# Kernel optimization log

Measured on AMD Instinct MI355X. Metric: run time of the kernel, lower is better.

## Reference

```python
import jax, jax.numpy as jnp
import numpy as np

N = 100_000   # nodes
D = 128       # in_size == out_size
E = 800_000   # edges per etype
NE = 2        # number of edge types
H = 4         # num_heads
HD = D // H   # head size
EPS = 1e-5


def setup_inputs() -> dict:
    key = jax.random.key(0)
    ks = jax.random.split(key, 10)
    s = 0.05
    return {
        "feat": jax.random.normal(ks[0], (N, D), jnp.float32),
        "src": jax.random.randint(ks[1], (NE, E), 0, N, dtype=jnp.int32),
        "dst": jax.random.randint(ks[2], (NE, E), 0, N, dtype=jnp.int32),
        # per-etype Linear weights stored [in, out] so y = x @ W + b (torch stores transposed)
        "Wt": jax.random.normal(ks[3], (NE, D, D), jnp.float32) * s,
        "bt": jnp.zeros((NE, D), jnp.float32),
        "Kw": jax.random.normal(ks[4], (NE, D, D), jnp.float32) * s,
        "Kb": jnp.zeros((NE, D), jnp.float32),
        "Qw": jax.random.normal(ks[5], (NE, D, D), jnp.float32) * s,
        "Qb": jnp.zeros((NE, D), jnp.float32),
        "Vw": jax.random.normal(ks[6], (NE, D, D), jnp.float32) * s,
        "Vb": jnp.zeros((NE, D), jnp.float32),
        "ln_g": jnp.ones((D,), jnp.float32),
        "ln_b": jnp.zeros((D,), jnp.float32),
    }


def _attn(Wh, kw, kb, qw, qb, vw, vb):
    # per-node multi-head attention ACROSS HEADS: attn is [N, H, H] (faithful to bmm in torch code)
    k = (Wh @ kw + kb).reshape(-1, H, HD)
    q = (Wh @ qw + qb).reshape(-1, H, HD)
    v = (Wh @ vw + vb).reshape(-1, H, HD)
    scores = jnp.einsum('nhd,ngd->nhg', q, k) / np.float32(np.sqrt(HD))
    a = jax.nn.softmax(scores, axis=2)  # dropout is identity in eval
    return jnp.einsum('nhg,ngd->nhd', a, v).reshape(-1, D)


def reference(feat, src, dst, Wt, bt, Kw, Kb, Qw, Qb, Vw, Vb, ln_g, ln_b):
    h = jnp.zeros_like(feat)
    ones_e = jnp.ones((E,), feat.dtype)
    for e in range(NE):  # small fixed loop over edge types
        Wh = _attn(feat @ Wt[e] + bt[e], Kw[e], Kb[e], Qw[e], Qb[e], Vw[e], Vb[e])
        msg = Wh[src[e]]                                      # copy_u: [E, D]
        tot = jax.ops.segment_sum(msg, dst[e], num_segments=N)
        deg = jax.ops.segment_sum(ones_e, dst[e], num_segments=N)
        h = h + tot / jnp.maximum(deg, 1.0)[:, None]          # mean (0 for isolated), cross-etype 'sum'
    h = h + feat  # identity residual (in_size == out_size)
    mu = jnp.mean(h, axis=-1, keepdims=True)
    var = jnp.mean((h - mu) ** 2, axis=-1, keepdims=True)
    return (h - mu) / jnp.sqrt(var + EPS) * ln_g + ln_b  # LayerNorm; dropout identity in eval
```

## Files before the change

### kernel.cpp

```cpp
#include <hip/hip_runtime.h>
#include <hip/hip_bf16.h>
#include <stdint.h>

#define D 128
#define NET 2
#define CAP 32

typedef __bf16 bf16x8 __attribute__((ext_vector_type(8)));
typedef float f32x4 __attribute__((ext_vector_type(4)));
typedef short s16x8 __attribute__((ext_vector_type(8)));
typedef unsigned short us16x8 __attribute__((ext_vector_type(8)));

__device__ __forceinline__ float b2f(unsigned short u) {
  return __builtin_bit_cast(float, ((uint32_t)u) << 16);
}
__device__ __forceinline__ unsigned short f2b(float f) {
  __hip_bfloat16 h = __float2bfloat16(f);
  return __builtin_bit_cast(unsigned short, h);
}

__global__ void k_combine(const float* __restrict__ Wt, const float* __restrict__ bt,
                          const float* __restrict__ Kw, const float* __restrict__ Kb,
                          const float* __restrict__ Qw, const float* __restrict__ Qb,
                          const float* __restrict__ Vw, const float* __restrict__ Vb,
                          unsigned short* __restrict__ WTc, float* __restrict__ bc) {
  int combo = blockIdx.y;
  int et = combo / 3, which = combo % 3;
  const float* W0 = Wt + (size_t)et * D * D;
  const float* W1 = ((which == 0) ? Kw : (which == 1) ? Qw : Vw) + (size_t)et * D * D;
  const float* b1 = ((which == 0) ? Kb : (which == 1) ? Qb : Vb) + (size_t)et * D;
  const float* b0 = bt + (size_t)et * D;

  int t = threadIdx.x;
  int i = blockIdx.x * 16 + (t >> 4);
  int jb = (t & 15) * 8;
  float acc[8];
#pragma unroll
  for (int j = 0; j < 8; j++) acc[j] = 0.f;
  for (int k = 0; k < D; k++) {
    float a0 = W0[(size_t)i * D + k];
    const float* w1p = W1 + (size_t)k * D + jb;
#pragma unroll
    for (int j = 0; j < 8; j++) acc[j] += a0 * w1p[j];
  }
  unsigned short* wout = WTc + (size_t)combo * D * D;
#pragma unroll
  for (int j = 0; j < 8; j++) wout[(size_t)(jb + j) * D + i] = f2b(acc[j]);

  if (blockIdx.x == 0 && t < D) {
    float s = b1[t];
    for (int k = 0; k < D; k++) s += b0[k] * W1[(size_t)k * D + t];
    bc[(size_t)combo * D + t] = s;
  }
}

__device__ __forceinline__ void stage_w(const unsigned short* __restrict__ W,
                                        unsigned short (*Ws)[136], int tid) {
  int r = tid >> 1, hh = tid & 1;
  const us16x8* gp = (const us16x8*)(W + (size_t)r * D + hh * 64);
  us16x8* lp = (us16x8*)&Ws[r][hh * 64];
#pragma unroll
  for (int i = 0; i < 8; i++) lp[i] = gp[i];
}

__device__ __forceinline__ void load_pf(const unsigned short* __restrict__ W,
                                        us16x8* pf, int sr, int sh) {
  const us16x8* gp = (const us16x8*)(W + (size_t)sr * D + sh * 64);
#pragma unroll
  for (int i = 0; i < 8; i++) pf[i] = gp[i];
}

__device__ __forceinline__ void write_pf(const us16x8* pf, unsigned short (*Ws)[136],
                                         int sr, int sh) {
  us16x8* lp = (us16x8*)&Ws[sr][sh * 64];
#pragma unroll
  for (int i = 0; i < 8; i++) lp[i] = pf[i];
}

__device__ __forceinline__ void gemm_frag(const bf16x8* af, unsigned short (*Ws)[136],
                                          int m, int q, f32x4* acc) {
#pragma unroll
  for (int nt = 0; nt < 8; nt++) {
    f32x4 a = {0.f, 0.f, 0.f, 0.f};
#pragma unroll
    for (int ks = 0; ks < 4; ks++) {
      s16x8 br = *(const s16x8*)&Ws[nt * 16 + m][ks * 32 + q * 8];
      a = __builtin_amdgcn_mfma_f32_16x16x32_bf16(af[ks], __builtin_bit_cast(bf16x8, br), a, 0, 0, 0);
    }
    acc[nt] = a;
  }
}

__global__ __launch_bounds__(256) void k_fused(
    const float* __restrict__ feat, const unsigned short* __restrict__ WTc,
    const float* __restrict__ bc, unsigned short* __restrict__ Whall, int nrows,
    const int* __restrict__ src, const int* __restrict__ dst,
    int* __restrict__ cnt, int* __restrict__ bucket, int Eper) {
  __shared__ unsigned short As[64][136];
  __shared__ unsigned short Ws[128][136];
  int tid = threadIdx.x;
  int bid = blockIdx.x;

  int ng = (nrows + 63) >> 6;
  int nE2 = NET * Eper;
  int nb = (nE2 + 1023) >> 10;
  int mmin = (ng < nb) ? ng : nb;
  int role, id;
  if (bid < 2 * mmin) { role = bid & 1; id = bid >> 1; }
  else {
    int left = bid - 2 * mmin;
    role = (ng > nb) ? 0 : 1;
    id = mmin + left;
  }

  if (role == 1) {
    int base = id << 10;
    int idx[4]; int dd[4]; int ss[4]; bool vld[4];
#pragma unroll
    for (int u = 0; u < 4; u++) {
      idx[u] = base + (u << 8) + tid;
      vld[u] = idx[u] < nE2;
      int j = vld[u] ? idx[u] : 0;
      dd[u] = dst[j];
      ss[u] = src[j];
    }
    int key[4]; int slot[4];
#pragma unroll
    for (int u = 0; u < 4; u++) {
      int et = (idx[u] >= Eper) ? 1 : 0;
      key[u] = et * nrows + dd[u];
      slot[u] = 0;
      if (vld[u]) slot[u] = atomicAdd(&cnt[key[u]], 1);
    }
#pragma unroll
    for (int u = 0; u < 4; u++) {
      int et = (idx[u] >= Eper) ? 1 : 0;
      if (vld[u] && slot[u] < CAP)
        bucket[(size_t)key[u] * CAP + slot[u]] = ss[u] + et * nrows;
    }
    return;
  }

  int row0 = id * 64;
  int w = tid >> 6, lane = tid & 63;
  int m = lane & 15, q = lane >> 4;

  {
    int r = tid >> 2, qq = tid & 3;
    int gr = row0 + r;
    unsigned short tmp[32];
    if (gr < nrows) {
      const f32x4* gp = (const f32x4*)(feat + (size_t)gr * D + qq * 32);
#pragma unroll
      for (int i = 0; i < 8; i++) {
        f32x4 v = gp[i];
#pragma unroll
        for (int j = 0; j < 4; j++) tmp[i * 4 + j] = f2b(v[j]);
      }
    } else {
#pragma unroll
      for (int i = 0; i < 32; i++) tmp[i] = 0;
    }
    us16x8* lp = (us16x8*)&As[r][qq * 32];
#pragma unroll
    for (int i = 0; i < 4; i++) lp[i] = *(const us16x8*)&tmp[i * 8];
  }
  stage_w(WTc, Ws, tid);
  __syncthreads();

  bf16x8 af[4];
#pragma unroll
  for (int ks = 0; ks < 4; ks++)
    af[ks] = __builtin_bit_cast(bf16x8, *(const s16x8*)&As[w * 16 + m][ks * 32 + q * 8]);

  int sr = tid >> 1, sh = tid & 1;
  us16x8 pf[8];
  load_pf(WTc + (size_t)1 * D * D, pf, sr, sh);

  const float scale = 0.17677669529663687f;

#pragma unroll
  for (int et = 0; et < NET; et++) {
    f32x4 acc[3][8];
#pragma unroll
    for (int which = 0; which < 3; which++) {
      const int combo = et * 3 + which;
      gemm_frag(af, Ws, m, q, acc[which]);
      const float* bb = bc + (size_t)combo * D;
#pragma unroll
      for (int nt = 0; nt < 8; nt++) acc[which][nt] += bb[nt * 16 + m];
      if (combo < 5) {
        __syncthreads();
        write_pf(pf, Ws, sr, sh);
        if (combo < 4)
          load_pf(WTc + (size_t)(combo + 2) * D * D, pf, sr, sh);
        __syncthreads();
      }
    }

    f32x4* kacc = acc[0];
    f32x4* qacc = acc[1];
    f32x4* vacc = acc[2];
    unsigned short* Wh = Whall + (size_t)et * nrows * D;
#pragma unroll
    for (int r = 0; r < 4; r++) {
      float sc[4][4];
#pragma unroll
      for (int hh = 0; hh < 4; hh++)
#pragma unroll
        for (int gg = 0; gg < 4; gg++)
          sc[hh][gg] = qacc[2 * hh][r] * kacc[2 * gg][r] + qacc[2 * hh + 1][r] * kacc[2 * gg + 1][r];
#pragma unroll
      for (int off = 1; off < 16; off <<= 1)
#pragma unroll
        for (int hh = 0; hh < 4; hh++)
#pragma unroll
          for (int gg = 0; gg < 4; gg++)
            sc[hh][gg] += __shfl_xor(sc[hh][gg], off, 64);
      float a[4][4];
#pragma unroll
      for (int hh = 0; hh < 4; hh++) {
        float s0 = sc[hh][0] * scale, s1 = sc[hh][1] * scale;
        float s2 = sc[hh][2] * scale, s3 = sc[hh][3] * scale;
        float mx = fmaxf(fmaxf(s0, s1), fmaxf(s2, s3));
        float e0 = __expf(s0 - mx), e1 = __expf(s1 - mx);
        float e2 = __expf(s2 - mx), e3 = __expf(s3 - mx);
        float inv = 1.f / (e0 + e1 + e2 + e3);
        a[hh][0] = e0 * inv; a[hh][1] = e1 * inv; a[hh][2] = e2 * inv; a[hh][3] = e3 * inv;
      }
      int grow = row0 + w * 16 + q * 4 + r;
      if (grow < nrows) {
        unsigned short* op = Wh + (size_t)grow * D;
#pragma unroll
        for (int nt = 0; nt < 8; nt++) {
          int hh = nt >> 1, lo = nt & 1;
          float o = a[hh][0] * vacc[0 + lo][r] + a[hh][1] * vacc[2 + lo][r] +
                    a[hh][2] * vacc[4 + lo][r] + a[hh][3] * vacc[6 + lo][r];
          op[nt * 16 + m] = f2b(o);
        }
      }
    }
  }
}

__global__ __launch_bounds__(256) void k_gather_ln(
    const unsigned short* __restrict__ Whall, const int* __restrict__ bucket,
    const int* __restrict__ cnt, const float* __restrict__ feat,
    const float* __restrict__ g, const float* __restrict__ b,
    float* __restrict__ out, int n) {
  int lane = threadIdx.x & 63, wv = threadIdx.x >> 6;
  int node = blockIdx.x * 4 + wv;
  if (node >= n) return;

  int c0 = cnt[node], c1 = cnt[n + node];
  int c0c = min(c0, CAP), c1c = min(c1, CAP);
  float w0 = 1.0f / fmaxf((float)c0, 1.0f);
  float w1 = 1.0f / fmaxf((float)c1, 1.0f);

  const float2* fp = (const float2*)(feat + (size_t)node * D);
  float2 fv = fp[lane];

  int myid = 0;
  if (lane < 32) {
    if (lane < c0c) myid = bucket[(size_t)node * CAP + lane];
  } else {
    if (lane - 32 < c1c) myid = bucket[((size_t)n + node) * CAP + (lane - 32)];
  }

  float a0 = 0.f, a1 = 0.f;
  for (int j = 0; j < c0c; j += 8) {
    int sid[8]; float wt[8];
#pragma unroll
    for (int u = 0; u < 8; u++) {
      int jj = j + u;
      bool v = jj < c0c;
      sid[u] = __shfl(myid, v ? jj : 0, 64);
      wt[u] = v ? w0 : 0.f;
    }
    ushort2 vv[8];
#pragma unroll
    for (int u = 0; u < 8; u++)
      vv[u] = *(const ushort2*)(Whall + (size_t)sid[u] * D + 2 * lane);
#pragma unroll
    for (int u = 0; u < 8; u++) {
      a0 += wt[u] * b2f(vv[u].x);
      a1 += wt[u] * b2f(vv[u].y);
    }
  }
  for (int j = 0; j < c1c; j += 8) {
    int sid[8]; float wt[8];
#pragma unroll
    for (int u = 0; u < 8; u++) {
      int jj = j + u;
      bool v = jj < c1c;
      sid[u] = __shfl(myid, v ? 32 + jj : 32, 64);
      wt[u] = v ? w1 : 0.f;
    }
    ushort2 vv[8];
#pragma unroll
    for (int u = 0; u < 8; u++)
      vv[u] = *(const ushort2*)(Whall + (size_t)sid[u] * D + 2 * lane);
#pragma unroll
    for (int u = 0; u < 8; u++) {
      a0 += wt[u] * b2f(vv[u].x);
      a1 += wt[u] * b2f(vv[u].y);
    }
  }

  float x0 = a0 + fv.x;
  float x1 = a1 + fv.y;

  float s = x0 + x1, s2 = x0 * x0 + x1 * x1;
#pragma unroll
  for (int off = 32; off > 0; off >>= 1) {
    s += __shfl_xor(s, off, 64);
    s2 += __shfl_xor(s2, off, 64);
  }
  float mu = s * (1.0f / 128.0f);
  float var = fmaxf(s2 * (1.0f / 128.0f) - mu * mu, 0.0f);
  float rs = rsqrtf(var + 1e-5f);

  float2 gv = ((const float2*)g)[lane];
  float2 bv = ((const float2*)b)[lane];
  float2 ov;
  ov.x = (x0 - mu) * rs * gv.x + bv.x;
  ov.y = (x1 - mu) * rs * gv.y + bv.y;
  ((float2*)(out + (size_t)node * D))[lane] = ov;
}

extern "C" void kernel_launch(void* const* d_in, const int* in_sizes, int n_in,
                              void* d_out, int out_size, void* d_ws, size_t ws_size,
                              hipStream_t stream) {
  const float* feat = (const float*)d_in[0];
  const int* src = (const int*)d_in[1];
  const int* dst = (const int*)d_in[2];
  const float* Wt = (const float*)d_in[3];
  const float* bt = (const float*)d_in[4];
  const float* Kw = (const float*)d_in[5];
  const float* Kb = (const float*)d_in[6];
  const float* Qw = (const float*)d_in[7];
  const float* Qb = (const float*)d_in[8];
  const float* Vw = (const float*)d_in[9];
  const float* Vb = (const float*)d_in[10];
  const float* lng = (const float*)d_in[11];
  const float* lnb = (const float*)d_in[12];

  const int N = in_sizes[0] / D;
  const int E = in_sizes[1] / NET;

  char* p = (char*)d_ws;
  unsigned short* Whall = (unsigned short*)p;  p += (size_t)NET * N * D * 2;
  int* bucket = (int*)p;                       p += (size_t)NET * N * CAP * sizeof(int);
  int* cnt = (int*)p;                          p += (size_t)NET * N * sizeof(int);
  unsigned short* WTc = (unsigned short*)p;    p += (size_t)NET * 3 * D * D * 2;
  float* bc = (float*)p;

  hipMemsetAsync(cnt, 0, (size_t)NET * N * sizeof(int), stream);
  k_combine<<<dim3(8, NET * 3), 256, 0, stream>>>(Wt, bt, Kw, Kb, Qw, Qb, Vw, Vb, WTc, bc);

  int ng = (N + 63) / 64;
  int nb = (NET * E + 1023) / 1024;
  k_fused<<<ng + nb, 256, 0, stream>>>(feat, WTc, bc, Whall, N, src, dst, cnt, bucket, E);

  k_gather_ln<<<(N + 3) / 4, 256, 0, stream>>>(Whall, bucket, cnt, feat, lng, lnb,
                                               (float*)d_out, N);
}
```

Measured before the change: 377.1 us.

## Use fixed persistent edge-bucketing blocks and pad degree counters to reduce contention

The fused kernel no longer interleaves one-shot edge-bucketing blocks with GEMM blocks. The first 128 blocks now each loop over a contiguous chunk of edges, processing 8 per thread per iteration, and the remaining blocks do the per-node attention GEMM. Degree counters are spaced 4 ints apart so that atomics on neighbouring nodes touch different 16-byte segments, which may reduce atomic contention. In exchange the counter array and its memset are four times larger, and with only 128 build blocks the bucketing may become a serial tail if those blocks finish after the GEMM blocks.

```diff
diff --git a/kernel.cpp b/kernel.cpp
--- a/kernel.cpp
+++ b/kernel.cpp
@@ -5,6 +5,8 @@
 #define D 128
 #define NET 2
 #define CAP 32
+#define CSTR 4
+#define NB_BUILD 128
 
 typedef __bf16 bf16x8 __attribute__((ext_vector_type(8)));
 typedef float f32x4 __attribute__((ext_vector_type(4)));
@@ -101,46 +103,40 @@
   int tid = threadIdx.x;
   int bid = blockIdx.x;
 
-  int ng = (nrows + 63) >> 6;
-  int nE2 = NET * Eper;
-  int nb = (nE2 + 1023) >> 10;
-  int mmin = (ng < nb) ? ng : nb;
-  int role, id;
-  if (bid < 2 * mmin) { role = bid & 1; id = bid >> 1; }
-  else {
-    int left = bid - 2 * mmin;
-    role = (ng > nb) ? 0 : 1;
-    id = mmin + left;
-  }
-
-  if (role == 1) {
-    int base = id << 10;
-    int idx[4]; int dd[4]; int ss[4]; bool vld[4];
-#pragma unroll
-    for (int u = 0; u < 4; u++) {
-      idx[u] = base + (u << 8) + tid;
-      vld[u] = idx[u] < nE2;
-      int j = vld[u] ? idx[u] : 0;
-      dd[u] = dst[j];
-      ss[u] = src[j];
-    }
-    int key[4]; int slot[4];
-#pragma unroll
-    for (int u = 0; u < 4; u++) {
-      int et = (idx[u] >= Eper) ? 1 : 0;
-      key[u] = et * nrows + dd[u];
-      slot[u] = 0;
-      if (vld[u]) slot[u] = atomicAdd(&cnt[key[u]], 1);
-    }
-#pragma unroll
-    for (int u = 0; u < 4; u++) {
-      int et = (idx[u] >= Eper) ? 1 : 0;
-      if (vld[u] && slot[u] < CAP)
-        bucket[(size_t)key[u] * CAP + slot[u]] = ss[u] + et * nrows;
+  if (bid < NB_BUILD) {
+    int nE2 = NET * Eper;
+    int chunk = (nE2 + NB_BUILD - 1) / NB_BUILD;
+    int start = bid * chunk;
+    int end = start + chunk; if (end > nE2) end = nE2;
+    for (int j = start; j < end; j += 2048) {
+      int idx[8]; int dd[8]; int ss[8]; bool vld[8];
+#pragma unroll
+      for (int u = 0; u < 8; u++) {
+        idx[u] = j + (u << 8) + tid;
+        vld[u] = idx[u] < end;
+        int jj = vld[u] ? idx[u] : start;
+        dd[u] = dst[jj];
+        ss[u] = src[jj];
+      }
+      int key[8]; int slot[8];
+#pragma unroll
+      for (int u = 0; u < 8; u++) {
+        int et = (idx[u] >= Eper) ? 1 : 0;
+        key[u] = et * nrows + dd[u];
+        slot[u] = CAP;
+        if (vld[u]) slot[u] = atomicAdd(&cnt[(size_t)key[u] * CSTR], 1);
+      }
+#pragma unroll
+      for (int u = 0; u < 8; u++) {
+        int et = (idx[u] >= Eper) ? 1 : 0;
+        if (vld[u] && slot[u] < CAP)
+          bucket[(size_t)key[u] * CAP + slot[u]] = ss[u] + et * nrows;
+      }
     }
     return;
   }
 
+  int id = bid - NB_BUILD;
   int row0 = id * 64;
   int w = tid >> 6, lane = tid & 63;
   int m = lane & 15, q = lane >> 4;
@@ -252,7 +248,7 @@
   int node = blockIdx.x * 4 + wv;
   if (node >= n) return;
 
-  int c0 = cnt[node], c1 = cnt[n + node];
+  int c0 = cnt[(size_t)node * CSTR], c1 = cnt[(size_t)(n + node) * CSTR];
   int c0c = min(c0, CAP), c1c = min(c1, CAP);
   float w0 = 1.0f / fmaxf((float)c0, 1.0f);
   float w1 = 1.0f / fmaxf((float)c1, 1.0f);
@@ -351,16 +347,15 @@
   char* p = (char*)d_ws;
   unsigned short* Whall = (unsigned short*)p;  p += (size_t)NET * N * D * 2;
   int* bucket = (int*)p;                       p += (size_t)NET * N * CAP * sizeof(int);
-  int* cnt = (int*)p;                          p += (size_t)NET * N * sizeof(int);
+  int* cnt = (int*)p;                          p += (size_t)NET * N * CSTR * sizeof(int);
   unsigned short* WTc = (unsigned short*)p;    p += (size_t)NET * 3 * D * D * 2;
   float* bc = (float*)p;
 
-  hipMemsetAsync(cnt, 0, (size_t)NET * N * sizeof(int), stream);
+  hipMemsetAsync(cnt, 0, (size_t)NET * N * CSTR * sizeof(int), stream);
   k_combine<<<dim3(8, NET * 3), 256, 0, stream>>>(Wt, bt, Kw, Kb, Qw, Qb, Vw, Vb, WTc, bc);
 
   int ng = (N + 63) / 64;
-  int nb = (NET * E + 1023) / 1024;
-  k_fused<<<ng + nb, 256, 0, stream>>>(feat, WTc, bc, Whall, N, src, dst, cnt, bucket, E);
+  k_fused<<<NB_BUILD + ng, 256, 0, stream>>>(feat, WTc, bc, Whall, N, src, dst, cnt, bucket, E);
 
   k_gather_ln<<<(N + 3) / 4, 256, 0, stream>>>(Whall, bucket, cnt, feat, lng, lnb,
                                                (float*)d_out, N);
```

Result: faster. 337.1 us (-10.6%).
